# Kernel optimization log

Measured on AMD Instinct MI355X. Metric: run time of the kernel, lower is better.

## Reference

```python
import jax, jax.numpy as jnp
import numpy as np

N_CLASSES = 18

def setup_inputs() -> dict:
    key = jax.random.key(0)
    k1, k2 = jax.random.split(key)
    B = 2_000_000
    output = jax.random.normal(k1, (B, N_CLASSES), dtype=jnp.float32)
    labels_soft = jax.random.uniform(k2, (B, N_CLASSES), dtype=jnp.float32)
    return {"output": output, "labels_soft": labels_soft}

def reference(output, labels_soft):
    # Original: sum over classes of mean_b( CE(output, cls) * labels_soft[:, cls] )
    # = mean over batch of sum_c( -log_softmax(output)[b, c] * labels_soft[b, c] )
    logp = jax.nn.log_softmax(output, axis=-1)          # [B, C]
    per_row = -jnp.sum(logp * labels_soft, axis=-1)     # [B]
    return jnp.mean(per_row)
```

## Files before the change

kernel.cpp:

```cpp
#include <hip/hip_runtime.h>

#define NCLS   18
#define TROWS  128
#define TWORDS (TROWS * NCLS)
#define NF4    (TWORDS / 4)

#define REP9(F) F(0) F(1) F(2) F(3) F(4) F(5) F(6) F(7) F(8)

__global__ __launch_bounds__(256) void ce_soft_main(
    const float* __restrict__ logits,
    const float* __restrict__ labels,
    float* __restrict__ partial,
    int B)
{
    __shared__ float4 sX[4][NF4];
    __shared__ float4 sL[4][NF4];
    __shared__ float sWS[4];

    const int tid  = threadIdx.x;
    const int lane = tid & 63;
    const int wid  = tid >> 6;
    float4* bufX = &sX[wid][0];
    float4* bufL = &sL[wid][0];

    const int nTiles  = B / TROWS;
    const int wgid    = blockIdx.x * 4 + wid;
    const int wstride = gridDim.x * 4;

    float acc = 0.0f;

#define DECLP(i) float4 px##i, pl##i;
    REP9(DECLP)
#undef DECLP

    if (wgid < nTiles) {
        const float4* gx = (const float4*)(logits + (size_t)wgid * TWORDS) + lane;
        const float4* gl = (const float4*)(labels + (size_t)wgid * TWORDS) + lane;
#define LOADP(i) px##i = gx[64 * i]; pl##i = gl[64 * i];
        REP9(LOADP)
#undef LOADP
    }

    for (int t = wgid; t < nTiles; t += wstride) {
#define STX(i) bufX[64 * i + lane] = px##i;
        REP9(STX)
#undef STX
#define STL(i) bufL[64 * i + lane] = pl##i;
        REP9(STL)
#undef STL

        int tn = t + wstride;
        if (tn < nTiles) {
            const float4* gx = (const float4*)(logits + (size_t)tn * TWORDS) + lane;
            const float4* gl = (const float4*)(labels + (size_t)tn * TWORDS) + lane;
#define LOADP(i) px##i = gx[64 * i]; pl##i = gl[64 * i];
            REP9(LOADP)
#undef LOADP
        }

        const float4* rx = bufX + lane * 9;
#define RDX(i) float4 v##i = rx[i];
        REP9(RDX)
#undef RDX

        float mA = fmaxf(fmaxf(fmaxf(v0.x, v0.y), fmaxf(v0.z, v0.w)),
                   fmaxf(fmaxf(fmaxf(v1.x, v1.y), fmaxf(v1.z, v1.w)),
                   fmaxf(fmaxf(fmaxf(v2.x, v2.y), fmaxf(v2.z, v2.w)),
                   fmaxf(fmaxf(fmaxf(v3.x, v3.y), fmaxf(v3.z, v3.w)),
                         fmaxf(v4.x, v4.y)))));
        float mB = fmaxf(fmaxf(fmaxf(v5.x, v5.y), fmaxf(v5.z, v5.w)),
                   fmaxf(fmaxf(fmaxf(v6.x, v6.y), fmaxf(v6.z, v6.w)),
                   fmaxf(fmaxf(fmaxf(v7.x, v7.y), fmaxf(v7.z, v7.w)),
                   fmaxf(fmaxf(fmaxf(v8.x, v8.y), fmaxf(v8.z, v8.w)),
                         fmaxf(v4.z, v4.w)))));

        float seA = __expf(v0.x - mA) + __expf(v0.y - mA) + __expf(v0.z - mA) + __expf(v0.w - mA)
                  + __expf(v1.x - mA) + __expf(v1.y - mA) + __expf(v1.z - mA) + __expf(v1.w - mA)
                  + __expf(v2.x - mA) + __expf(v2.y - mA) + __expf(v2.z - mA) + __expf(v2.w - mA)
                  + __expf(v3.x - mA) + __expf(v3.y - mA) + __expf(v3.z - mA) + __expf(v3.w - mA)
                  + __expf(v4.x - mA) + __expf(v4.y - mA);
        float seB = __expf(v4.z - mB) + __expf(v4.w - mB)
                  + __expf(v5.x - mB) + __expf(v5.y - mB) + __expf(v5.z - mB) + __expf(v5.w - mB)
                  + __expf(v6.x - mB) + __expf(v6.y - mB) + __expf(v6.z - mB) + __expf(v6.w - mB)
                  + __expf(v7.x - mB) + __expf(v7.y - mB) + __expf(v7.z - mB) + __expf(v7.w - mB)
                  + __expf(v8.x - mB) + __expf(v8.y - mB) + __expf(v8.z - mB) + __expf(v8.w - mB);

        float lseA = mA + __logf(seA);
        float lseB = mB + __logf(seB);

        const float4* rl = bufL + lane * 9;
        {
            float4 w;
            w = rl[0];
            acc = fmaf(w.x, lseA - v0.x, acc); acc = fmaf(w.y, lseA - v0.y, acc);
            acc = fmaf(w.z, lseA - v0.z, acc); acc = fmaf(w.w, lseA - v0.w, acc);
            w = rl[1];
            acc = fmaf(w.x, lseA - v1.x, acc); acc = fmaf(w.y, lseA - v1.y, acc);
            acc = fmaf(w.z, lseA - v1.z, acc); acc = fmaf(w.w, lseA - v1.w, acc);
            w = rl[2];
            acc = fmaf(w.x, lseA - v2.x, acc); acc = fmaf(w.y, lseA - v2.y, acc);
            acc = fmaf(w.z, lseA - v2.z, acc); acc = fmaf(w.w, lseA - v2.w, acc);
            w = rl[3];
            acc = fmaf(w.x, lseA - v3.x, acc); acc = fmaf(w.y, lseA - v3.y, acc);
            acc = fmaf(w.z, lseA - v3.z, acc); acc = fmaf(w.w, lseA - v3.w, acc);
            w = rl[4];
            acc = fmaf(w.x, lseA - v4.x, acc); acc = fmaf(w.y, lseA - v4.y, acc);
            acc = fmaf(w.z, lseB - v4.z, acc); acc = fmaf(w.w, lseB - v4.w, acc);
            w = rl[5];
            acc = fmaf(w.x, lseB - v5.x, acc); acc = fmaf(w.y, lseB - v5.y, acc);
            acc = fmaf(w.z, lseB - v5.z, acc); acc = fmaf(w.w, lseB - v5.w, acc);
            w = rl[6];
            acc = fmaf(w.x, lseB - v6.x, acc); acc = fmaf(w.y, lseB - v6.y, acc);
            acc = fmaf(w.z, lseB - v6.z, acc); acc = fmaf(w.w, lseB - v6.w, acc);
            w = rl[7];
            acc = fmaf(w.x, lseB - v7.x, acc); acc = fmaf(w.y, lseB - v7.y, acc);
            acc = fmaf(w.z, lseB - v7.z, acc); acc = fmaf(w.w, lseB - v7.w, acc);
            w = rl[8];
            acc = fmaf(w.x, lseB - v8.x, acc); acc = fmaf(w.y, lseB - v8.y, acc);
            acc = fmaf(w.z, lseB - v8.z, acc); acc = fmaf(w.w, lseB - v8.w, acc);
        }
    }

    for (int row = nTiles * TROWS + blockIdx.x * blockDim.x + tid; row < B;
         row += gridDim.x * blockDim.x) {
        const float2* o2 = (const float2*)(logits + (size_t)row * NCLS);
        const float2* l2 = (const float2*)(labels + (size_t)row * NCLS);
        float x[NCLS], l[NCLS];
        #pragma unroll
        for (int k = 0; k < NCLS / 2; ++k) {
            float2 v = o2[k]; x[2 * k] = v.x; x[2 * k + 1] = v.y;
            float2 w = l2[k]; l[2 * k] = w.x; l[2 * k + 1] = w.y;
        }
        float mm = x[0];
        #pragma unroll
        for (int c = 1; c < NCLS; ++c) mm = fmaxf(mm, x[c]);
        float se = 0.f, dot = 0.f, sl = 0.f;
        #pragma unroll
        for (int c = 0; c < NCLS; ++c) {
            se += __expf(x[c] - mm);
            dot = fmaf(l[c], x[c], dot);
            sl += l[c];
        }
        acc = fmaf(sl, mm + __logf(se), acc - dot);
    }

    #pragma unroll
    for (int off = 32; off > 0; off >>= 1)
        acc += __shfl_down(acc, off, 64);
    if (lane == 0) sWS[wid] = acc;
    __syncthreads();
    if (tid == 0)
        partial[blockIdx.x] = sWS[0] + sWS[1] + sWS[2] + sWS[3];
}

__global__ __launch_bounds__(256) void ce_soft_finish(
    const float* __restrict__ partial, float* __restrict__ result,
    int n, float invB)
{
    float s = 0.f;
    for (int i = threadIdx.x; i < n; i += 256) s += partial[i];
    #pragma unroll
    for (int off = 32; off > 0; off >>= 1)
        s += __shfl_down(s, off, 64);
    __shared__ float ws[4];
    int lane = threadIdx.x & 63, wid = threadIdx.x >> 6;
    if (lane == 0) ws[wid] = s;
    __syncthreads();
    if (threadIdx.x == 0)
        result[0] = (ws[0] + ws[1] + ws[2] + ws[3]) * invB;
}

extern "C" void kernel_launch(void* const* d_in, const int* in_sizes, int n_in,
                              void* d_out, int out_size, void* d_ws, size_t ws_size,
                              hipStream_t stream) {
    const float* logits = (const float*)d_in[0];
    const float* labels = (const float*)d_in[1];
    float* result = (float*)d_out;

    int B = in_sizes[0] / NCLS;

    int grid = 512;
    if (ws_size < (size_t)grid * sizeof(float)) {
        grid = (int)(ws_size / sizeof(float));
        if (grid > 512) grid = 512;
        if (grid < 1) grid = 1;
    }
    float* partial = (float*)d_ws;

    ce_soft_main<<<grid, 256, 0, stream>>>(logits, labels, partial, B);
    ce_soft_finish<<<1, 256, 0, stream>>>(partial, result, grid, 1.0f / (float)B);
}
```

Before: 295.9 us.

## Double register prefetch to keep two tiles of loads in flight per wave

Switches the per-wave loop from single-tile register prefetch to two register sets (A/B), so each wave keeps loads for the next two tiles outstanding while computing the current one. The aim is more memory-level parallelism on this bandwidth-bound streaming reduction. The compute body moves into a macro, and launch bounds now request 2 blocks per SIMD. The extra 72 float4 registers raise register pressure and may reduce occupancy or cause spills.

```diff
diff --git a/kernel.cpp b/kernel.cpp
--- a/kernel.cpp
+++ b/kernel.cpp
@@ -7,7 +7,65 @@
 
 #define REP9(F) F(0) F(1) F(2) F(3) F(4) F(5) F(6) F(7) F(8)
 
-__global__ __launch_bounds__(256) void ce_soft_main(
+#define COMPUTE_TILE()                                                                   \
+  do {                                                                                   \
+    const float4* rx = bufX + lane * 9;     \
+    float4 v0 = rx[0], v1 = rx[1], v2 = rx[2], v3 = rx[3], v4 = rx[4],                   \
+           v5 = rx[5], v6 = rx[6], v7 = rx[7], v8 = rx[8];                               \
+    float mA = fmaxf(fmaxf(fmaxf(v0.x, v0.y), fmaxf(v0.z, v0.w)),                        \
+               fmaxf(fmaxf(fmaxf(v1.x, v1.y), fmaxf(v1.z, v1.w)),                        \
+               fmaxf(fmaxf(fmaxf(v2.x, v2.y), fmaxf(v2.z, v2.w)),                        \
+               fmaxf(fmaxf(fmaxf(v3.x, v3.y), fmaxf(v3.z, v3.w)),                        \
+                     fmaxf(v4.x, v4.y)))));                                              \
+    float mB = fmaxf(fmaxf(fmaxf(v5.x, v5.y), fmaxf(v5.z, v5.w)),                        \
+               fmaxf(fmaxf(fmaxf(v6.x, v6.y), fmaxf(v6.z, v6.w)),                        \
+               fmaxf(fmaxf(fmaxf(v7.x, v7.y), fmaxf(v7.z, v7.w)),                        \
+               fmaxf(fmaxf(fmaxf(v8.x, v8.y), fmaxf(v8.z, v8.w)),                        \
+                     fmaxf(v4.z, v4.w)))));                                              \
+    float seA = __expf(v0.x-mA)+__expf(v0.y-mA)+__expf(v0.z-mA)+__expf(v0.w-mA)          \
+              + __expf(v1.x-mA)+__expf(v1.y-mA)+__expf(v1.z-mA)+__expf(v1.w-mA)          \
+              + __expf(v2.x-mA)+__expf(v2.y-mA)+__expf(v2.z-mA)+__expf(v2.w-mA)          \
+              + __expf(v3.x-mA)+__expf(v3.y-mA)+__expf(v3.z-mA)+__expf(v3.w-mA)          \
+              + __expf(v4.x-mA)+__expf(v4.y-mA);                                         \
+    float seB = __expf(v4.z-mB)+__expf(v4.w-mB)                                          \
+              + __expf(v5.x-mB)+__expf(v5.y-mB)+__expf(v5.z-mB)+__expf(v5.w-mB)          \
+              + __expf(v6.x-mB)+__expf(v6.y-mB)+__expf(v6.z-mB)+__expf(v6.w-mB)          \
+              + __expf(v7.x-mB)+__expf(v7.y-mB)+__expf(v7.z-mB)+__expf(v7.w-mB)          \
+              + __expf(v8.x-mB)+__expf(v8.y-mB)+__expf(v8.z-mB)+__expf(v8.w-mB);         \
+    float lseA = mA + __logf(seA);                                                       \
+    float lseB = mB + __logf(seB);                                                       \
+    const float4* rl = bufL + lane * 9;                                                  \
+    float4 w;                                                                            \
+    w = rl[0];                                                                           \
+    acc = fmaf(w.x, lseA - v0.x, acc); acc = fmaf(w.y, lseA - v0.y, acc);                \
+    acc = fmaf(w.z, lseA - v0.z, acc); acc = fmaf(w.w, lseA - v0.w, acc);                \
+    w = rl[1];                                                                           \
+    acc = fmaf(w.x, lseA - v1.x, acc); acc = fmaf(w.y, lseA - v1.y, acc);                \
+    acc = fmaf(w.z, lseA - v1.z, acc); acc = fmaf(w.w, lseA - v1.w, acc);                \
+    w = rl[2];                                                                           \
+    acc = fmaf(w.x, lseA - v2.x, acc); acc = fmaf(w.y, lseA - v2.y, acc);                \
+    acc = fmaf(w.z, lseA - v2.z, acc); acc = fmaf(w.w, lseA - v2.w, acc);                \
+    w = rl[3];                                                                           \
+    acc = fmaf(w.x, lseA - v3.x, acc); acc = fmaf(w.y, lseA - v3.y, acc);                \
+    acc = fmaf(w.z, lseA - v3.z, acc); acc = fmaf(w.w, lseA - v3.w, acc);                \
+    w = rl[4];                                                                           \
+    acc = fmaf(w.x, lseA - v4.x, acc); acc = fmaf(w.y, lseA - v4.y, acc);                \
+    acc = fmaf(w.z, lseB - v4.z, acc); acc = fmaf(w.w, lseB - v4.w, acc);                \
+    w = rl[5];                                                                           \
+    acc = fmaf(w.x, lseB - v5.x, acc); acc = fmaf(w.y, lseB - v5.y, acc);                \
+    acc = fmaf(w.z, lseB - v5.z, acc); acc = fmaf(w.w, lseB - v5.w, acc);                \
+    w = rl[6];                                                                           \
+    acc = fmaf(w.x, lseB - v6.x, acc); acc = fmaf(w.y, lseB - v6.y, acc);                \
+    acc = fmaf(w.z, lseB - v6.z, acc); acc = fmaf(w.w, lseB - v6.w, acc);                \
+    w = rl[7];                                                                           \
+    acc = fmaf(w.x, lseB - v7.x, acc); acc = fmaf(w.y, lseB - v7.y, acc);                \
+    acc = fmaf(w.z, lseB - v7.z, acc); acc = fmaf(w.w, lseB - v7.w, acc);                \
+    w = rl[8];                                                                           \
+    acc = fmaf(w.x, lseB - v8.x, acc); acc = fmaf(w.y, lseB - v8.y, acc);                \
+    acc = fmaf(w.z, lseB - v8.z, acc); acc = fmaf(w.w, lseB - v8.w, acc);                \
+  } while (0)
+
+__global__ __launch_bounds__(256, 2) void ce_soft_main(
     const float* __restrict__ logits,
     const float* __restrict__ labels,
     float* __restrict__ partial,
@@ -29,97 +87,62 @@
 
     float acc = 0.0f;
 
-#define DECLP(i) float4 px##i, pl##i;
+#define DECLP(i) float4 Ax##i, Al##i, Bx##i, Bl##i;
     REP9(DECLP)
 #undef DECLP
+
+#define LOADA(i) Ax##i = gx[64 * i]; Al##i = gl[64 * i];
+#define LOADB(i) Bx##i = gx[64 * i]; Bl##i = gl[64 * i];
 
     if (wgid < nTiles) {
         const float4* gx = (const float4*)(logits + (size_t)wgid * TWORDS) + lane;
         const float4* gl = (const float4*)(labels + (size_t)wgid * TWORDS) + lane;
-#define LOADP(i) px##i = gx[64 * i]; pl##i = gl[64 * i];
-        REP9(LOADP)
-#undef LOADP
-    }
-
-    for (int t = wgid; t < nTiles; t += wstride) {
-#define STX(i) bufX[64 * i + lane] = px##i;
-        REP9(STX)
-#undef STX
-#define STL(i) bufL[64 * i + lane] = pl##i;
-        REP9(STL)
-#undef STL
-
-        int tn = t + wstride;
-        if (tn < nTiles) {
-            const float4* gx = (const float4*)(logits + (size_t)tn * TWORDS) + lane;
-            const float4* gl = (const float4*)(labels + (size_t)tn * TWORDS) + lane;
-#define LOADP(i) px##i = gx[64 * i]; pl##i = gl[64 * i];
-            REP9(LOADP)
-#undef LOADP
-        }
-
-        const float4* rx = bufX + lane * 9;
-#define RDX(i) float4 v##i = rx[i];
-        REP9(RDX)
-#undef RDX
-
-        float mA = fmaxf(fmaxf(fmaxf(v0.x, v0.y), fmaxf(v0.z, v0.w)),
-                   fmaxf(fmaxf(fmaxf(v1.x, v1.y), fmaxf(v1.z, v1.w)),
-                   fmaxf(fmaxf(fmaxf(v2.x, v2.y), fmaxf(v2.z, v2.w)),
-                   fmaxf(fmaxf(fmaxf(v3.x, v3.y), fmaxf(v3.z, v3.w)),
-                         fmaxf(v4.x, v4.y)))));
-        float mB = fmaxf(fmaxf(fmaxf(v5.x, v5.y), fmaxf(v5.z, v5.w)),
-                   fmaxf(fmaxf(fmaxf(v6.x, v6.y), fmaxf(v6.z, v6.w)),
-                   fmaxf(fmaxf(fmaxf(v7.x, v7.y), fmaxf(v7.z, v7.w)),
-                   fmaxf(fmaxf(fmaxf(v8.x, v8.y), fmaxf(v8.z, v8.w)),
-                         fmaxf(v4.z, v4.w)))));
-
-        float seA = __expf(v0.x - mA) + __expf(v0.y - mA) + __expf(v0.z - mA) + __expf(v0.w - mA)
-                  + __expf(v1.x - mA) + __expf(v1.y - mA) + __expf(v1.z - mA) + __expf(v1.w - mA)
-                  + __expf(v2.x - mA) + __expf(v2.y - mA) + __expf(v2.z - mA) + __expf(v2.w - mA)
-                  + __expf(v3.x - mA) + __expf(v3.y - mA) + __expf(v3.z - mA) + __expf(v3.w - mA)
-                  + __expf(v4.x - mA) + __expf(v4.y - mA);
-        float seB = __expf(v4.z - mB) + __expf(v4.w - mB)
-                  + __expf(v5.x - mB) + __expf(v5.y - mB) + __expf(v5.z - mB) + __expf(v5.w - mB)
-                  + __expf(v6.x - mB) + __expf(v6.y - mB) + __expf(v6.z - mB) + __expf(v6.w - mB)
-                  + __expf(v7.x - mB) + __expf(v7.y - mB) + __expf(v7.z - mB) + __expf(v7.w - mB)
-                  + __expf(v8.x - mB) + __expf(v8.y - mB) + __expf(v8.z - mB) + __expf(v8.w - mB);
-
-        float lseA = mA + __logf(seA);
-        float lseB = mB + __logf(seB);
-
-        const float4* rl = bufL + lane * 9;
+        REP9(LOADA)
+    }
+    if (wgid + wstride < nTiles) {
+        const float4* gx = (const float4*)(logits + (size_t)(wgid + wstride) * TWORDS) + lane;
+        const float4* gl = (const float4*)(labels + (size_t)(wgid + wstride) * TWORDS) + lane;
+        REP9(LOADB)
+    }
+
+    for (int t = wgid; t < nTiles; t += 2 * wstride) {
+#define STXA(i) bufX[64 * i + lane] = Ax##i;
+#define STLA(i) bufL[64 * i + lane] = Al##i;
+        REP9(STXA)
+        REP9(STLA)
+#undef STXA
+#undef STLA
         {
-            float4 w;
-            w = rl[0];
-            acc = fmaf(w.x, lseA - v0.x, acc); acc = fmaf(w.y, lseA - v0.y, acc);
-            acc = fmaf(w.z, lseA - v0.z, acc); acc = fmaf(w.w, lseA - v0.w, acc);
-            w = rl[1];
-            acc = fmaf(w.x, lseA - v1.x, acc); acc = fmaf(w.y, lseA - v1.y, acc);
-            acc = fmaf(w.z, lseA - v1.z, acc); acc = fmaf(w.w, lseA - v1.w, acc);
-            w = rl[2];
-            acc = fmaf(w.x, lseA - v2.x, acc); acc = fmaf(w.y, lseA - v2.y, acc);
-            acc = fmaf(w.z, lseA - v2.z, acc); acc = fmaf(w.w, lseA - v2.w, acc);
-            w = rl[3];
-            acc = fmaf(w.x, lseA - v3.x, acc); acc = fmaf(w.y, lseA - v3.y, acc);
-            acc = fmaf(w.z, lseA - v3.z, acc); acc = fmaf(w.w, lseA - v3.w, acc);
-            w = rl[4];
-            acc = fmaf(w.x, lseA - v4.x, acc); acc = fmaf(w.y, lseA - v4.y, acc);
-            acc = fmaf(w.z, lseB - v4.z, acc); acc = fmaf(w.w, lseB - v4.w, acc);
-            w = rl[5];
-            acc = fmaf(w.x, lseB - v5.x, acc); acc = fmaf(w.y, lseB - v5.y, acc);
-            acc = fmaf(w.z, lseB - v5.z, acc); acc = fmaf(w.w, lseB - v5.w, acc);
-            w = rl[6];
-            acc = fmaf(w.x, lseB - v6.x, acc); acc = fmaf(w.y, lseB - v6.y, acc);
-            acc = fmaf(w.z, lseB - v6.z, acc); acc = fmaf(w.w, lseB - v6.w, acc);
-            w = rl[7];
-            acc = fmaf(w.x, lseB - v7.x, acc); acc = fmaf(w.y, lseB - v7.y, acc);
-            acc = fmaf(w.z, lseB - v7.z, acc); acc = fmaf(w.w, lseB - v7.w, acc);
-            w = rl[8];
-            acc = fmaf(w.x, lseB - v8.x, acc); acc = fmaf(w.y, lseB - v8.y, acc);
-            acc = fmaf(w.z, lseB - v8.z, acc); acc = fmaf(w.w, lseB - v8.w, acc);
-        }
-    }
+            int tn = t + 2 * wstride;
+            if (tn < nTiles) {
+                const float4* gx = (const float4*)(logits + (size_t)tn * TWORDS) + lane;
+                const float4* gl = (const float4*)(labels + (size_t)tn * TWORDS) + lane;
+                REP9(LOADA)
+            }
+        }
+        COMPUTE_TILE();
+
+        int t1 = t + wstride;
+        if (t1 < nTiles) {
+#define STXB(i) bufX[64 * i + lane] = Bx##i;
+#define STLB(i) bufL[64 * i + lane] = Bl##i;
+            REP9(STXB)
+            REP9(STLB)
+#undef STXB
+#undef STLB
+            {
+                int tn = t1 + 2 * wstride;
+                if (tn < nTiles) {
+                    const float4* gx = (const float4*)(logits + (size_t)tn * TWORDS) + lane;
+                    const float4* gl = (const float4*)(labels + (size_t)tn * TWORDS) + lane;
+                    REP9(LOADB)
+                }
+            }
+            COMPUTE_TILE();
+        }
+    }
+#undef LOADA
+#undef LOADB
 
     for (int row = nTiles * TROWS + blockIdx.x * blockDim.x + tid; row < B;
          row += gridDim.x * blockDim.x) {
```

New measurement: 296.6 us. Within noise of the previous version (+0.2%).
